# Optimization experiments

Hardware: AMD Instinct MI355X
Metric: run time of the kernel (lower is better)

Reference implementation:

```python
import jax, jax.numpy as jnp
import numpy as np

EPS = 1e-7
INF = 1e8
NUM_CLASSES = 80
SOFT_CENTER_RADIUS = 3.0
TOPK = 13
IOU_WEIGHT = 3.0
ALPHA = 1.0
BETA = 6.0
IMG = 640.0


def pairwise_iou(b1, b2):
    # b1: (B,N,4), b2: (B,M,4) in xyxy -> (B,N,M) IoU (mmdet BboxOverlaps2D, eps=1e-6)
    a1 = (b1[..., 2] - b1[..., 0]) * (b1[..., 3] - b1[..., 1])
    a2 = (b2[..., 2] - b2[..., 0]) * (b2[..., 3] - b2[..., 1])
    lt = jnp.maximum(b1[:, :, None, :2], b2[:, None, :, :2])
    rb = jnp.minimum(b1[:, :, None, 2:], b2[:, None, :, 2:])
    wh = jnp.clip(rb - lt, 0.0)
    inter = wh[..., 0] * wh[..., 1]
    union = a1[:, :, None] + a2[:, None, :] - inter
    return inter / jnp.maximum(union, 1e-6)


def _forward(pred_bboxes, pred_scores, priors, gt_labels, gt_bboxes, pad_bbox_flag):
    B, P, _ = pred_bboxes.shape
    G = gt_bboxes.shape[1]
    dt = pred_bboxes.dtype
    labels = gt_labels[..., 0]            # (B,G) int
    pad = pad_bbox_flag[..., 0]           # (B,G) float
    prior_xy = priors[:, :2]              # (P,2)
    strides = priors[:, 2]                # (P,)

    # ---- inside-gt test (find_inside_points, box_dim=4): (B,P,G) bool
    lt_ = prior_xy[None, :, None, :] - gt_bboxes[:, None, :, :2]
    rb_ = gt_bboxes[:, None, :, 2:] - prior_xy[None, :, None, :]
    is_in_gts = jnp.minimum(lt_.min(-1), rb_.min(-1)) > 0        # (B,P,G)
    is_in_gts_f = is_in_gts.astype(dt) * pad[:, None, :]         # masked by pad flag
    valid_mask = is_in_gts_f.sum(-1) > 0                          # (B,P)

    # ---- get_pos_mask (TaskAligned metric top-k) -> fg_mask_pre_prior
    overlaps = pairwise_iou(gt_bboxes, pred_bboxes)               # (B,G,P)
    scores_sig = jax.nn.sigmoid(pred_scores)                      # (B,P,C)
    scores_g = jnp.take_along_axis(scores_sig.transpose(0, 2, 1), labels[:, :, None], axis=1)  # (B,G,P)
    align = (scores_g ** ALPHA) * (overlaps ** BETA)              # (B,G,P)
    in_gts_gp = is_in_gts.transpose(0, 2, 1).astype(dt)           # (B,G,P)
    metrics = align * in_gts_gp
    _, topk_idxs = jax.lax.top_k(metrics, TOPK)                   # (B,G,TOPK)
    bb = jnp.arange(B)[:, None, None]
    gg = jnp.arange(G)[None, :, None]
    cnt = jnp.zeros((B, G, P), dt).at[bb, gg, topk_idxs].add(1.0)
    cnt = cnt * pad[:, :, None]
    is_in_topk = jnp.where(cnt > 1, 0.0, cnt)
    pos_mask = is_in_topk * in_gts_gp * pad[:, :, None]           # (B,G,P)
    # select_highest_overlaps: resolve priors matched to >1 gt via max IoU
    fg_pre = pos_mask.sum(1)                                      # (B,P)
    max_gt = overlaps.argmax(1)                                   # (B,P)
    is_max = (jnp.arange(G)[None, None, :] == max_gt[:, :, None]).astype(dt)  # (B,P,G)
    pos_mask = jnp.where((fg_pre > 1)[:, None, :], is_max.transpose(0, 2, 1), pos_mask)
    fg_mask_pre_prior = pos_mask.sum(1) > 0                       # (B,P) bool

    # ---- soft center prior
    gt_center = (gt_bboxes[..., :2] + gt_bboxes[..., 2:]) / 2.0   # (B,G,2)
    dist = jnp.sqrt(((prior_xy[None, :, None, :] - gt_center[:, None, :, :]) ** 2).sum(-1)) \
           / strides[None, :, None]                               # (B,P,G)
    dist = dist * valid_mask[..., None]
    soft_center_prior = jnp.power(10.0, dist - SOFT_CENTER_RADIUS)

    # ---- IoU cost
    pairwise_ious = pairwise_iou(pred_bboxes, gt_bboxes)          # (B,P,G)
    iou_cost = -jnp.log(pairwise_ious + EPS) * IOU_WEIGHT

    # ---- soft classification cost (QFL-style)
    logits = jnp.take_along_axis(pred_scores.transpose(0, 2, 1), labels[:, :, None], axis=1)
    logits = logits.transpose(0, 2, 1)                            # (B,P,G)
    scale = pairwise_ious - jax.nn.sigmoid(logits)
    bce = jnp.logaddexp(0.0, logits) - logits * pairwise_ious     # BCEWithLogits(logits, ious)
    cls_cost = bce * scale ** 2

    cost = cls_cost + iou_cost + soft_center_prior
    cost = jnp.where(valid_mask[..., None], cost, INF)            # (B,P,G)

    # ---- dynamic-k matching
    topk_ious, _ = jax.lax.top_k(pairwise_ious.transpose(0, 2, 1), TOPK)  # (B,G,TOPK)
    dynamic_ks = jnp.maximum(topk_ious.sum(-1).astype(jnp.int32), 1)      # (B,G)
    num_gts = pad.sum(-1).astype(jnp.int32)                                # (B,)
    sorted_idx = jnp.argsort(cost, axis=1)                                 # (B,P,G)
    ranks = jnp.arange(P)[None, :, None]
    gt_valid = jnp.arange(G)[None, :] < num_gts[:, None]                   # (B,G)
    sel = (ranks < dynamic_ks[:, None, :]) & gt_valid[:, None, :]          # (B,P,G), in sorted order
    bb2 = jnp.arange(B)[:, None, None]
    gg2 = jnp.arange(G)[None, None, :]
    matching = jnp.zeros((B, P, G), dt).at[bb2, sorted_idx, gg2].set(sel.astype(dt))
    multi = matching.sum(-1) > 1                                           # (B,P)
    argmin = cost.argmin(-1)                                               # (B,P)
    onehot_min = (jnp.arange(G)[None, None, :] == argmin[:, :, None]).astype(dt)
    matching = jnp.where(multi[..., None], onehot_min, matching)
    fg = matching.sum(-1) > 0                                              # (B,P)
    matched_ious = (matching * pairwise_ious).sum(-1)                      # (B,P)
    matched_gt_inds = matching.argmax(-1)                                  # (B,P)

    # ---- dense outputs (torch scatters into full-size tensors; same values here)
    assigned_labels = jnp.where(fg, jnp.take_along_axis(labels, matched_gt_inds, axis=1), NUM_CLASSES)
    assigned_labels_weights = jnp.ones((B, P), dt)
    assigned_bboxes = jnp.where(fg[..., None],
                                jnp.take_along_axis(gt_bboxes, matched_gt_inds[..., None].repeat(4, -1), axis=1),
                                0.0)
    assign_metrics = jnp.where(fg, matched_ious, 0.0)
    return assigned_labels, assigned_labels_weights, assigned_bboxes, assign_metrics, fg_mask_pre_prior


def setup_inputs() -> dict:
    key = jax.random.key(0)
    ks = jax.random.split(key, 6)
    B, G, C = 16, 100, 80
    # priors: anchor-free grid for 640x640, strides (8,16,32) -> P = 8400
    grids = []
    for s in (8, 16, 32):
        n = 640 // s
        xs = (np.arange(n, dtype=np.float32) + 0.5) * s
        yy, xx = np.meshgrid(xs, xs, indexing='ij')
        g = np.stack([xx.ravel(), yy.ravel(),
                      np.full(n * n, s, np.float32), np.full(n * n, s, np.float32)], -1)
        grids.append(g)
    priors = jnp.asarray(np.concatenate(grids, 0), jnp.float32)  # (8400, 4)
    P = priors.shape[0]

    def rand_boxes(k, shape):
        kc, kw = jax.random.split(k)
        cxy = jax.random.uniform(kc, shape + (2,), minval=0.0, maxval=IMG)
        wh = jax.random.uniform(kw, shape + (2,), minval=8.0, maxval=256.0)
        lt = jnp.clip(cxy - wh / 2, 0.0, IMG)
        rb = jnp.clip(cxy + wh / 2, 0.0, IMG)
        return jnp.concatenate([lt, rb], -1)

    pred_bboxes = rand_boxes(ks[0], (B, P))
    pred_scores = jax.random.normal(ks[1], (B, P, C), jnp.float32) * 2.0 - 2.0
    gt_bboxes = rand_boxes(ks[2], (B, G))
    gt_labels = jax.random.randint(ks[3], (B, G, 1), 0, C)
    n_valid = jax.random.randint(ks[4], (B,), 1, G + 1)
    pad_bbox_flag = (jnp.arange(G)[None, :] < n_valid[:, None]).astype(jnp.float32)[..., None]
    return {"pred_bboxes": pred_bboxes, "pred_scores": pred_scores, "priors": priors,
            "gt_labels": gt_labels, "gt_bboxes": gt_bboxes, "pad_bbox_flag": pad_bbox_flag}


def reference(pred_bboxes, pred_scores, priors, gt_labels, gt_bboxes, pad_bbox_flag):
    return _forward(pred_bboxes, pred_scores, priors, gt_labels, gt_bboxes, pad_bbox_flag)
```

## Files before the change

kernel.cpp:

```cpp
#include <hip/hip_runtime.h>
#include <cstdint>
#include <climits>
#include <cstddef>

#define TK 13
#define MAXG 128
#define CAP 192
#define NW 4
#define MCAP 24576

__device__ __forceinline__ float iou_fn(const float4 pb, const float4 gb){
  float pa = (pb.z - pb.x) * (pb.w - pb.y);
  float ga = (gb.z - gb.x) * (gb.w - gb.y);
  float ltx = fmaxf(pb.x, gb.x), lty = fmaxf(pb.y, gb.y);
  float rbx = fminf(pb.z, gb.z), rby = fminf(pb.w, gb.w);
  float w = fmaxf(rbx - ltx, 0.0f), h = fmaxf(rby - lty, 0.0f);
  float inter = w * h;
  float uni = pa + ga - inter;
  return inter / fmaxf(uni, 1e-6f);
}

__device__ __forceinline__ float sigmoid_f(float x){ return 1.0f / (1.0f + expf(-x)); }

__device__ __forceinline__ float cost_full(float iou, float s, float dist){
  float sig = sigmoid_f(s);
  float iouc = -logf(iou + 1e-7f) * 3.0f;
  float scale = iou - sig;
  float bce = fmaxf(s, 0.0f) + log1pf(expf(-fabsf(s))) - s * iou;
  float cls = bce * scale * scale;
  float soft = powf(10.0f, dist - 3.0f);
  return cls + iouc + soft;
}

__device__ __forceinline__ void bfly_max_u64(unsigned long long &v, int &l){
  #pragma unroll
  for (int off = 32; off >= 1; off >>= 1){
    unsigned long long ov = __shfl_xor(v, off);
    int ol = __shfl_xor(l, off);
    if (ov > v){ v = ov; l = ol; }
  }
}

__device__ __forceinline__ unsigned long long squeeze13(unsigned long long* buf, int& cnt, int lane){
  unsigned long long e0 = (lane < cnt) ? buf[lane] : 0ull;
  unsigned long long e1 = (lane + 64 < cnt) ? buf[lane + 64] : 0ull;
  unsigned long long e2 = (lane + 128 < cnt) ? buf[lane + 128] : 0ull;
  if (e0 < e2){ unsigned long long t = e0; e0 = e2; e2 = t; }
  if (e0 < e1){ unsigned long long t = e0; e0 = e1; e1 = t; }
  if (e1 < e2){ unsigned long long t = e1; e1 = e2; e2 = t; }
  unsigned long long T = 0;
  for (int r = 0; r < TK; ++r){
    unsigned long long m = e0; int l = lane;
    bfly_max_u64(m, l);
    if (lane == 0) buf[r] = m;
    T = m;
    if (lane == l){ e0 = e1; e1 = e2; e2 = 0ull; }
  }
  cnt = TK;
  return T;
}

__global__ __launch_bounds__(256) void k_valid(
    const float4* __restrict__ priors, const float4* __restrict__ gtb,
    const float* __restrict__ pad, unsigned long long* __restrict__ vmask,
    unsigned int* __restrict__ acc, unsigned int* __restrict__ mcnt,
    int P, int G, int nCh)
{
  int b = blockIdx.y;
  int p = blockIdx.x * 256 + threadIdx.x;
  if (b == 0 && p == 0) *mcnt = 0u;
  __shared__ float4 sg[MAXG];
  __shared__ float sp[MAXG];
  for (int i = threadIdx.x; i < G; i += 256){ sg[i] = gtb[b*G + i]; sp[i] = pad[b*G + i]; }
  __syncthreads();
  if (p >= P) return;
  float4 pr = priors[p];
  bool v = false;
  #pragma unroll 4
  for (int g = 0; g < G; ++g){
    float4 gb = sg[g];
    bool ig = (pr.x > gb.x) && (pr.y > gb.y) && (gb.z > pr.x) && (gb.w > pr.y);
    v = v || (ig && sp[g] > 0.5f);
  }
  size_t o = (size_t)b * P + p;
  acc[o] = 0u;
  unsigned long long m = __ballot(v);
  if ((threadIdx.x & 63) == 0) vmask[(size_t)b * nCh + (p >> 6)] = m;
}

__global__ __launch_bounds__(256) void k_scan(
    const float4* __restrict__ pred_bboxes, const float* __restrict__ pred_scores,
    const float4* __restrict__ priors, const int* __restrict__ gt_labels,
    const float4* __restrict__ gtbb, const float* __restrict__ pad,
    const unsigned long long* __restrict__ vmask,
    unsigned int* __restrict__ acc, unsigned int* __restrict__ mcnt,
    unsigned int* __restrict__ mlist,
    int P, int G, int C, int nCh)
{
  int bg = blockIdx.x;
  if (pad[bg] <= 0.5f) return;
  int b = bg / G;
  int g = bg - b * G;
  int tid = threadIdx.x;
  int lane = tid & 63;
  int wv = tid >> 6;
  float4 gb = gtbb[bg];
  int lbl = gt_labels[bg];
  float gcx = (gb.x + gb.z) * 0.5f, gcy = (gb.y + gb.w) * 0.5f;
  size_t bP = (size_t)b * P;
  const unsigned long long* vmb = vmask + (size_t)b * nCh;

  __shared__ unsigned long long bufM[NW*CAP], bufC[NW*CAP], bufI[NW*CAP];
  __shared__ unsigned int shwC, shwM, shwI;
  if (tid == 0){ shwC = 0xFFFFFFFFu; shwM = 0u; shwI = 0u; }
  __syncthreads();
  unsigned long long* bM = bufM + wv*CAP;
  unsigned long long* bC = bufC + wv*CAP;
  unsigned long long* bI = bufI + wv*CAP;

  int cntM = 0, cntC = 0, cntI = 0;
  int zM = 0, zC = 0;
  unsigned long long Tm = 0ull, Tc = 0ull;
  unsigned long long Ti = 0x00000000FFFFFFFFull;
  unsigned cbits = 0xFFFFFFFFu, mBbits = 0u, iBb = 0u;
  float thr = 1e30f, mB = 0.0f;
  unsigned long long laneLT = (1ull << lane) - 1ull;

  int p = wv * 64 + lane;
  bool inb = p < P;
  float4 pr = make_float4(0,0,0,0), pb = pr; bool vb = false;
  if (inb){
    pr = priors[p]; pb = pred_bboxes[bP + p]; vb = (vmb[wv] >> lane) & 1ull;
  }
  for (int c = wv; c < nCh; c += NW){
    int cn = c + NW;
    int pn = cn * 64 + lane;
    bool inbn = (cn < nCh) && (pn < P);
    float4 prn = make_float4(0,0,0,0), pbn = prn; bool vbn = false;
    if (inbn){
      prn = priors[pn]; pbn = pred_bboxes[bP + pn]; vbn = (vmb[cn] >> (pn & 63)) & 1ull;
    }
    { unsigned sC = shwC; if (sC < cbits){ cbits = sC;
        thr = 3.0f + log10f(__uint_as_float(cbits) * 1.00002f + 1e-6f); } }
    { unsigned sM = shwM; if (sM > mBbits){ mBbits = sM; mB = __uint_as_float(sM); } }
    { unsigned sI = shwI; if (sI > iBb) iBb = sI; }
    float iou = iou_fn(pb, gb);
    bool ig = inb && (pr.x > gb.x) && (pr.y > gb.y) && (gb.z > pr.x) && (gb.w > pr.y);
    bool pos = ig && (iou > 0.0f);
    unsigned long long keyI = ((unsigned long long)__float_as_uint(iou) << 32) | (unsigned)p;
    bool candI = inb && (keyI > Ti) && !((unsigned)(keyI >> 32) < iBb);
    float i2 = iou * iou;
    float bnd = (i2 * i2) * i2 * 1.000002f;
    bool needm = pos && !(bnd < mB);
    float dist = 0.0f; bool needc = false;
    if (vb){
      float dx = pr.x - gcx, dy = pr.y - gcy;
      dist = sqrtf(dx*dx + dy*dy) / pr.z;
      needc = !(dist > thr);
    }
    float sc = 0.0f;
    if (needm || needc) sc = pred_scores[(bP + p) * C + lbl];
    unsigned long long keyM = 0;
    if (__ballot(needm)){
      float met = sigmoid_f(sc) * powf(iou, 6.0f);
      if (needm)
        keyM = ((unsigned long long)__float_as_uint(met) << 32)
             | (unsigned)~(unsigned)((p << 1) | 1);
    }
    if (zM < TK && inb && !pos)
      keyM = (unsigned long long)(unsigned)~(unsigned)((p << 1) | (ig ? 1 : 0));
    bool candM = (keyM != 0ull) && (keyM > Tm) && !((unsigned)(keyM >> 32) < mBbits);
    unsigned long long keyC = 0;
    if (zC < TK && inb && !vb)
      keyC = ~(((unsigned long long)__float_as_uint(1e8f) << 32) | (unsigned)p);
    if (__ballot(needc)){
      float cst = cost_full(iou, sc, dist);
      if (needc)
        keyC = ~(((unsigned long long)__float_as_uint(cst) << 32) | (unsigned)p);
    }
    bool candC = (keyC != 0ull) && (keyC > Tc) && !((unsigned)((~keyC) >> 32) > cbits);
    if (cntI > CAP - 64){
      Ti = squeeze13(bI, cntI, lane);
      unsigned ib = (unsigned)(Ti >> 32);
      if (ib > iBb) iBb = ib;
      if (lane == 0 && ib) atomicMax(&shwI, ib);
      candI = candI && (keyI > Ti) && !((unsigned)(keyI >> 32) < iBb);
    }
    { unsigned long long mk = __ballot(candI);
      if (mk){ int off = cntI + __popcll(mk & laneLT); if (candI) bI[off] = keyI; cntI += __popcll(mk); } }
    if (cntM > CAP - 64){
      Tm = squeeze13(bM, cntM, lane);
      unsigned tb = (unsigned)(Tm >> 32);
      if (tb > mBbits){ mBbits = tb; mB = __uint_as_float(tb); }
      if (lane == 0 && tb) atomicMax(&shwM, tb);
      candM = candM && (keyM > Tm) && !((unsigned)(keyM >> 32) < mBbits);
    }
    { unsigned long long mk = __ballot(candM);
      if (mk){
        int off = cntM + __popcll(mk & laneLT);
        if (candM) bM[off] = keyM;
        cntM += __popcll(mk);
        unsigned long long zk = __ballot(candM && !pos);
        zM += __popcll(zk);
      } }
    if (cntC > CAP - 64){
      Tc = squeeze13(bC, cntC, lane);
      unsigned cb = (unsigned)((~Tc) >> 32);
      if (cb < cbits){ cbits = cb;
        thr = 3.0f + log10f(__uint_as_float(cbits) * 1.00002f + 1e-6f); }
      if (lane == 0) atomicMin(&shwC, cb);
      candC = candC && (keyC > Tc) && !((unsigned)((~keyC) >> 32) > cbits);
    }
    { unsigned long long mk = __ballot(candC);
      if (mk){
        int off = cntC + __popcll(mk & laneLT);
        if (candC) bC[off] = keyC;
        cntC += __popcll(mk);
        unsigned long long zk = __ballot(candC && !vb);
        zC += __popcll(zk);
      } }

    p = pn; inb = inbn; pr = prn; pb = pbn; vb = vbn;
  }

  squeeze13(bI, cntI, lane);
  squeeze13(bM, cntM, lane);
  squeeze13(bC, cntC, lane);
  __syncthreads();
  if (wv != 0) return;

  int w13 = lane / TK, r13 = lane - w13 * TK;
  int kd;
  {
    unsigned long long e = (lane < NW*TK) ? bufI[w13*CAP + r13] : 0ull;
    float ksum = 0.0f;
    for (int r = 0; r < TK; ++r){
      unsigned long long m = e; int l = lane;
      bfly_max_u64(m, l);
      ksum += __uint_as_float((unsigned)(m >> 32));
      if (lane == l) e = 0ull;
    }
    kd = (int)ksum; if (kd < 1) kd = 1;
  }
  {
    unsigned long long e = (lane < NW*TK) ? bufM[w13*CAP + r13] : 0ull;
    for (int r = 0; r < TK; ++r){
      unsigned long long m = e; int l = lane;
      bfly_max_u64(m, l);
      if (lane == 0 && m != 0ull){
        unsigned ix = ~(unsigned)(m & 0xFFFFFFFFull);
        if (ix & 1u) atomicOr(&acc[bP + (ix >> 1)], 2u);
      }
      if (lane == l) e = 0ull;
    }
  }
  {
    unsigned long long e = (lane < NW*TK) ? bufC[w13*CAP + r13] : 0ull;
    for (int r = 0; r < kd; ++r){
      unsigned long long m = e; int l = lane;
      bfly_max_u64(m, l);
      if (lane == 0 && m != 0ull){
        unsigned pp = (unsigned)((~m) & 0xFFFFFFFFull);
        unsigned old = atomicAdd(&acc[bP + pp], (1u << 17) | ((unsigned)g << 2));
        if ((old >> 17) == 1u){
          unsigned mi = atomicAdd(mcnt, 1u);
          if (mi < MCAP) mlist[mi] = (unsigned)(bP + pp);
        }
      }
      if (lane == l) e = 0ull;
    }
  }
}

__global__ __launch_bounds__(256) void k_final(
    const float4* __restrict__ pred_bboxes, const int* __restrict__ gt_labels,
    const float4* __restrict__ gtb, const unsigned int* __restrict__ acc,
    float* __restrict__ out, int B, int P, int G)
{
  int b = blockIdx.y;
  int p = blockIdx.x * 256 + threadIdx.x;
  __shared__ float4 sg[MAXG];
  __shared__ int sl[MAXG];
  for (int i = threadIdx.x; i < G; i += 256){
    sg[i] = gtb[b*G + i]; sl[i] = gt_labels[b*G + i];
  }
  __syncthreads();
  if (p >= P) return;
  size_t o = (size_t)b * P + p;
  unsigned int w = acc[o];
  int cnt = (int)(w >> 17);
  bool fg = cnt > 0;
  int mg = (cnt == 1) ? (int)((w >> 2) & 0x7FFFu) : 0;
  float4 pb = pred_bboxes[o];
  size_t BP = (size_t)B * P;
  out[o] = fg ? (float)sl[mg] : 80.0f;
  out[BP + o] = 1.0f;
  float4 ob = fg ? sg[mg] : make_float4(0.f, 0.f, 0.f, 0.f);
  ((float4*)(out + 2*BP))[o] = ob;
  out[6*BP + o] = fg ? iou_fn(pb, sg[mg]) : 0.0f;
  out[7*BP + o] = ((w >> 1) & 1u) ? 1.0f : 0.0f;
}

__global__ __launch_bounds__(256) void k_multi(
    const float4* __restrict__ pred_bboxes, const float* __restrict__ pred_scores,
    const float4* __restrict__ priors, const int* __restrict__ gt_labels,
    const float4* __restrict__ gtb, const unsigned long long* __restrict__ vmask,
    const unsigned int* __restrict__ mcnt, const unsigned int* __restrict__ mlist,
    float* __restrict__ out, int B, int P, int G, int C, int nCh)
{
  unsigned n = *mcnt; if (n > MCAP) n = MCAP;
  int lane = threadIdx.x & 63;
  int wid = (blockIdx.x * (blockDim.x >> 6)) + (threadIdx.x >> 6);
  int nw = gridDim.x * (blockDim.x >> 6);
  size_t BP = (size_t)B * P;
  for (unsigned i = wid; i < n; i += nw){
    unsigned o = mlist[i];
    int b = o / P;
    int p = o - b * P;
    float4 pb = pred_bboxes[o];
    bool vld = (vmask[(size_t)b * nCh + (p >> 6)] >> (p & 63)) & 1ull;
    int mg = 0;
    if (vld){
      float4 pr = priors[p];
      const float* srow = pred_scores + (size_t)o * C;
      unsigned long long best = 0xFFFFFFFFFFFFFFFFull;
      for (int g0 = lane; g0 < G; g0 += 64){
        float4 gbx = gtb[b*G + g0];
        float iou = iou_fn(pb, gbx);
        float s = srow[gt_labels[b*G + g0]];
        float gcx = (gbx.x + gbx.z) * 0.5f, gcy = (gbx.y + gbx.w) * 0.5f;
        float dx = pr.x - gcx, dy = pr.y - gcy;
        float dist = sqrtf(dx*dx + dy*dy) / pr.z;
        float cc = cost_full(iou, s, dist);
        unsigned long long k = ((unsigned long long)__float_as_uint(cc) << 32) | (unsigned)g0;
        if (k < best) best = k;
      }
      #pragma unroll
      for (int off = 32; off >= 1; off >>= 1){
        unsigned long long ov = __shfl_xor(best, off);
        if (ov < best) best = ov;
      }
      mg = (int)(best & 0xFFFFFFFFull);
    }
    if (lane == 0){
      float4 gbx = gtb[b*G + mg];
      out[o] = (float)gt_labels[b*G + mg];
      ((float4*)(out + 2*BP))[o] = gbx;
      out[6*BP + o] = iou_fn(pb, gbx);
    }
  }
}

extern "C" void kernel_launch(void* const* d_in, const int* in_sizes, int n_in,
                              void* d_out, int out_size, void* d_ws, size_t ws_size,
                              hipStream_t stream)
{
  const float4* pred_bboxes = (const float4*)d_in[0];
  const float*  pred_scores = (const float*)d_in[1];
  const float4* priors      = (const float4*)d_in[2];
  const int*    gt_labels   = (const int*)d_in[3];
  const float4* gt_bboxes   = (const float4*)d_in[4];
  const float*  pad         = (const float*)d_in[5];
  int P = in_sizes[2] / 4;
  int B = in_sizes[0] / (P * 4);
  int C = in_sizes[1] / (B * P);
  int G = in_sizes[4] / (B * 4);
  int BG = B * G;
  int nCh = (P + 63) >> 6;

  uint8_t* ws = (uint8_t*)d_ws;
  size_t accOff  = (size_t)B * nCh * 8;
  size_t mcntOff = accOff + (size_t)B * P * 4;
  mcntOff = (mcntOff + 15) & ~(size_t)15;
  size_t mlistOff = mcntOff + 16;

  unsigned long long* vmask = (unsigned long long*)ws;
  unsigned int* acc   = (unsigned int*)(ws + accOff);
  unsigned int* mcnt  = (unsigned int*)(ws + mcntOff);
  unsigned int* mlist = (unsigned int*)(ws + mlistOff);
  float* out = (float*)d_out;

  dim3 gridA((P + 255) / 256, B);
  k_valid<<<gridA, 256, 0, stream>>>(priors, gt_bboxes, pad, vmask, acc, mcnt, P, G, nCh);
  k_scan<<<BG, NW*64, 0, stream>>>(pred_bboxes, pred_scores,
                                   priors, gt_labels, gt_bboxes, pad, vmask,
                                   acc, mcnt, mlist, P, G, C, nCh);
  k_final<<<gridA, 256, 0, stream>>>(pred_bboxes, gt_labels, gt_bboxes, acc, out, B, P, G);
  k_multi<<<64, 256, 0, stream>>>(pred_bboxes, pred_scores, priors, gt_labels, gt_bboxes,
                                  vmask, mcnt, mlist, out, B, P, G, C, nCh);
}
```

Measured before the change: 275.8 us.

## Double waves per gt block in scan kernel and merge with two-candidate lanes

Raises the scan kernel's block to 512 threads (8 waves) so each gt's prior range is split across twice as many waves. The final top-k merge now holds two candidate entries per lane to cover the 8×13 partial results. Early break is added when no candidates remain. This aims to shorten the per-gt serial scan at the cost of larger blocks, more shared memory for the per-wave buffers, and a larger merge.

Result: slower. 297.3 us (+7.8%).

```diff
diff --git a/kernel.cpp b/kernel.cpp
--- a/kernel.cpp
+++ b/kernel.cpp
@@ -6,7 +6,7 @@
 #define TK 13
 #define MAXG 128
 #define CAP 192
-#define NW 4
+#define NW 8
 #define MCAP 24576
 
 __device__ __forceinline__ float iou_fn(const float4 pb, const float4 gb){
@@ -88,7 +88,7 @@
   if ((threadIdx.x & 63) == 0) vmask[(size_t)b * nCh + (p >> 6)] = m;
 }
 
-__global__ __launch_bounds__(256) void k_scan(
+__global__ __launch_bounds__(512) void k_scan(
     const float4* __restrict__ pred_bboxes, const float* __restrict__ pred_scores,
     const float4* __restrict__ priors, const int* __restrict__ gt_labels,
     const float4* __restrict__ gtbb, const float* __restrict__ pad,
@@ -229,37 +229,44 @@
   __syncthreads();
   if (wv != 0) return;
 
-  int w13 = lane / TK, r13 = lane - w13 * TK;
+  int i0 = lane, i1 = lane + 64;
+  int w0 = i0 / TK, r0 = i0 - w0 * TK;
+  int w1 = i1 / TK, r1 = i1 - w1 * TK;
   int kd;
   {
-    unsigned long long e = (lane < NW*TK) ? bufI[w13*CAP + r13] : 0ull;
+    unsigned long long e0 = (i0 < NW*TK) ? bufI[w0*CAP + r0] : 0ull;
+    unsigned long long e1 = (i1 < NW*TK) ? bufI[w1*CAP + r1] : 0ull;
     float ksum = 0.0f;
     for (int r = 0; r < TK; ++r){
-      unsigned long long m = e; int l = lane;
+      unsigned long long m = e0 > e1 ? e0 : e1; int l = lane;
       bfly_max_u64(m, l);
       ksum += __uint_as_float((unsigned)(m >> 32));
-      if (lane == l) e = 0ull;
+      if (lane == l){ if (e0 == m) e0 = 0ull; else e1 = 0ull; }
     }
     kd = (int)ksum; if (kd < 1) kd = 1;
   }
   {
-    unsigned long long e = (lane < NW*TK) ? bufM[w13*CAP + r13] : 0ull;
+    unsigned long long e0 = (i0 < NW*TK) ? bufM[w0*CAP + r0] : 0ull;
+    unsigned long long e1 = (i1 < NW*TK) ? bufM[w1*CAP + r1] : 0ull;
     for (int r = 0; r < TK; ++r){
-      unsigned long long m = e; int l = lane;
+      unsigned long long m = e0 > e1 ? e0 : e1; int l = lane;
       bfly_max_u64(m, l);
-      if (lane == 0 && m != 0ull){
+      if (m == 0ull) break;
+      if (lane == 0){
         unsigned ix = ~(unsigned)(m & 0xFFFFFFFFull);
         if (ix & 1u) atomicOr(&acc[bP + (ix >> 1)], 2u);
       }
-      if (lane == l) e = 0ull;
+      if (lane == l){ if (e0 == m) e0 = 0ull; else e1 = 0ull; }
     }
   }
   {
-    unsigned long long e = (lane < NW*TK) ? bufC[w13*CAP + r13] : 0ull;
+    unsigned long long e0 = (i0 < NW*TK) ? bufC[w0*CAP + r0] : 0ull;
+    unsigned long long e1 = (i1 < NW*TK) ? bufC[w1*CAP + r1] : 0ull;
     for (int r = 0; r < kd; ++r){
-      unsigned long long m = e; int l = lane;
+      unsigned long long m = e0 > e1 ? e0 : e1; int l = lane;
       bfly_max_u64(m, l);
-      if (lane == 0 && m != 0ull){
+      if (m == 0ull) break;
+      if (lane == 0){
         unsigned pp = (unsigned)((~m) & 0xFFFFFFFFull);
         unsigned old = atomicAdd(&acc[bP + pp], (1u << 17) | ((unsigned)g << 2));
         if ((old >> 17) == 1u){
@@ -267,7 +274,7 @@
           if (mi < MCAP) mlist[mi] = (unsigned)(bP + pp);
         }
       }
-      if (lane == l) e = 0ull;
+      if (lane == l){ if (e0 == m) e0 = 0ull; else e1 = 0ull; }
     }
   }
 }
```

## Skip whole prior chunks via per-chunk bounding boxes; fold multi-assign into final kernel

Applied to the files above, without the earlier changes.

k_valid now also stores a per-64-prior bounding box of the predicted boxes and of the prior centres, plus the chunk stride. k_scan uses these boxes to skip whole chunks that cannot overlap the gt box or fall below the current top-k cost and metric thresholds, so it loads fewer predictions, priors and scores. The separate k_multi kernel and its global list are removed. Priors matched to several gts are resolved in k_final with a nearest-centre seed and a lower-bound prune on the distance cost. This adds bound computations and more divergent work in k_final, and relies on the pruning bounds being conservative.

After: 362.1 us. +31.3%, slower.

```diff
diff --git a/kernel.cpp b/kernel.cpp
--- a/kernel.cpp
+++ b/kernel.cpp
@@ -7,7 +7,6 @@
 #define MAXG 128
 #define CAP 192
 #define NW 4
-#define MCAP 24576
 
 __device__ __forceinline__ float iou_fn(const float4 pb, const float4 gb){
   float pa = (pb.z - pb.x) * (pb.w - pb.y);
@@ -61,31 +60,51 @@
 }
 
 __global__ __launch_bounds__(256) void k_valid(
-    const float4* __restrict__ priors, const float4* __restrict__ gtb,
-    const float* __restrict__ pad, unsigned long long* __restrict__ vmask,
-    unsigned int* __restrict__ acc, unsigned int* __restrict__ mcnt,
+    const float4* __restrict__ priors, const float4* __restrict__ pred_bboxes,
+    const float4* __restrict__ gtb, const float* __restrict__ pad,
+    unsigned long long* __restrict__ vmask, unsigned int* __restrict__ acc,
+    float4* __restrict__ predAB, float4* __restrict__ prAB, float* __restrict__ strC,
     int P, int G, int nCh)
 {
   int b = blockIdx.y;
   int p = blockIdx.x * 256 + threadIdx.x;
-  if (b == 0 && p == 0) *mcnt = 0u;
   __shared__ float4 sg[MAXG];
   __shared__ float sp[MAXG];
   for (int i = threadIdx.x; i < G; i += 256){ sg[i] = gtb[b*G + i]; sp[i] = pad[b*G + i]; }
   __syncthreads();
-  if (p >= P) return;
-  float4 pr = priors[p];
+  int lane = threadIdx.x & 63;
+  int ch = p >> 6;
+  bool inb = p < P;
+  float4 pr = inb ? priors[p] : make_float4(0,0,0,0);
+  float4 pb = inb ? pred_bboxes[(size_t)b*P + p] : make_float4(0,0,0,0);
   bool v = false;
-  #pragma unroll 4
-  for (int g = 0; g < G; ++g){
-    float4 gb = sg[g];
-    bool ig = (pr.x > gb.x) && (pr.y > gb.y) && (gb.z > pr.x) && (gb.w > pr.y);
-    v = v || (ig && sp[g] > 0.5f);
-  }
-  size_t o = (size_t)b * P + p;
-  acc[o] = 0u;
+  if (inb){
+    #pragma unroll 4
+    for (int g = 0; g < G; ++g){
+      float4 gb = sg[g];
+      bool ig = (pr.x > gb.x) && (pr.y > gb.y) && (gb.z > pr.x) && (gb.w > pr.y);
+      v = v || (ig && sp[g] > 0.5f);
+    }
+    acc[(size_t)b * P + p] = 0u;
+  }
   unsigned long long m = __ballot(v);
-  if ((threadIdx.x & 63) == 0) vmask[(size_t)b * nCh + (p >> 6)] = m;
+  if (lane == 0 && ch < nCh) vmask[(size_t)b * nCh + ch] = m;
+  float inf = __builtin_inff();
+  float x1 = inb ? pb.x : inf,  y1 = inb ? pb.y : inf;
+  float x2 = inb ? pb.z : -inf, y2 = inb ? pb.w : -inf;
+  float px1 = inb ? pr.x : inf,  py1 = inb ? pr.y : inf;
+  float px2 = inb ? pr.x : -inf, py2 = inb ? pr.y : -inf;
+  #pragma unroll
+  for (int off = 32; off >= 1; off >>= 1){
+    x1 = fminf(x1, __shfl_xor(x1, off));  y1 = fminf(y1, __shfl_xor(y1, off));
+    x2 = fmaxf(x2, __shfl_xor(x2, off));  y2 = fmaxf(y2, __shfl_xor(y2, off));
+    px1 = fminf(px1, __shfl_xor(px1, off)); py1 = fminf(py1, __shfl_xor(py1, off));
+    px2 = fmaxf(px2, __shfl_xor(px2, off)); py2 = fmaxf(py2, __shfl_xor(py2, off));
+  }
+  if (lane == 0 && ch < nCh){
+    predAB[(size_t)b * nCh + ch] = make_float4(x1, y1, x2, y2);
+    if (b == 0){ prAB[ch] = make_float4(px1, py1, px2, py2); strC[ch] = pr.z; }
+  }
 }
 
 __global__ __launch_bounds__(256) void k_scan(
@@ -93,9 +112,9 @@
     const float4* __restrict__ priors, const int* __restrict__ gt_labels,
     const float4* __restrict__ gtbb, const float* __restrict__ pad,
     const unsigned long long* __restrict__ vmask,
-    unsigned int* __restrict__ acc, unsigned int* __restrict__ mcnt,
-    unsigned int* __restrict__ mlist,
-    int P, int G, int C, int nCh)
+    const float4* __restrict__ predAB, const float4* __restrict__ prAB,
+    const float* __restrict__ strC,
+    unsigned int* __restrict__ acc, int P, int G, int C, int nCh)
 {
   int bg = blockIdx.x;
   if (pad[bg] <= 0.5f) return;
@@ -109,6 +128,8 @@
   float gcx = (gb.x + gb.z) * 0.5f, gcy = (gb.y + gb.w) * 0.5f;
   size_t bP = (size_t)b * P;
   const unsigned long long* vmb = vmask + (size_t)b * nCh;
+  const float4* pAB = predAB + (size_t)b * nCh;
+  const unsigned B1E8 = __float_as_uint(1e8f);
 
   __shared__ unsigned long long bufM[NW*CAP], bufC[NW*CAP], bufI[NW*CAP];
   __shared__ unsigned int shwC, shwM, shwI;
@@ -126,101 +147,111 @@
   float thr = 1e30f, mB = 0.0f;
   unsigned long long laneLT = (1ull << lane) - 1ull;
 
-  int p = wv * 64 + lane;
-  bool inb = p < P;
-  float4 pr = make_float4(0,0,0,0), pb = pr; bool vb = false;
-  if (inb){
-    pr = priors[p]; pb = pred_bboxes[bP + p]; vb = (vmb[wv] >> lane) & 1ull;
-  }
+  float4 pA = pAB[wv];
+  float4 rA = prAB[wv];
+  float strc = strC[wv];
   for (int c = wv; c < nCh; c += NW){
     int cn = c + NW;
-    int pn = cn * 64 + lane;
-    bool inbn = (cn < nCh) && (pn < P);
-    float4 prn = make_float4(0,0,0,0), pbn = prn; bool vbn = false;
-    if (inbn){
-      prn = priors[pn]; pbn = pred_bboxes[bP + pn]; vbn = (vmb[cn] >> (pn & 63)) & 1ull;
-    }
+    float4 pAn = pA, rAn = rA; float strn = strc;
+    if (cn < nCh){ pAn = pAB[cn]; rAn = prAB[cn]; strn = strC[cn]; }
     { unsigned sC = shwC; if (sC < cbits){ cbits = sC;
         thr = 3.0f + log10f(__uint_as_float(cbits) * 1.00002f + 1e-6f); } }
     { unsigned sM = shwM; if (sM > mBbits){ mBbits = sM; mB = __uint_as_float(sM); } }
     { unsigned sI = shwI; if (sI > iBb) iBb = sI; }
-    float iou = iou_fn(pb, gb);
-    bool ig = inb && (pr.x > gb.x) && (pr.y > gb.y) && (gb.z > pr.x) && (gb.w > pr.y);
-    bool pos = ig && (iou > 0.0f);
-    unsigned long long keyI = ((unsigned long long)__float_as_uint(iou) << 32) | (unsigned)p;
-    bool candI = inb && (keyI > Ti) && !((unsigned)(keyI >> 32) < iBb);
-    float i2 = iou * iou;
-    float bnd = (i2 * i2) * i2 * 1.000002f;
-    bool needm = pos && !(bnd < mB);
-    float dist = 0.0f; bool needc = false;
-    if (vb){
-      float dx = pr.x - gcx, dy = pr.y - gcy;
-      dist = sqrtf(dx*dx + dy*dy) / pr.z;
-      needc = !(dist > thr);
-    }
-    float sc = 0.0f;
-    if (needm || needc) sc = pred_scores[(bP + p) * C + lbl];
-    unsigned long long keyM = 0;
-    if (__ballot(needm)){
-      float met = sigmoid_f(sc) * powf(iou, 6.0f);
-      if (needm)
-        keyM = ((unsigned long long)__float_as_uint(met) << 32)
-             | (unsigned)~(unsigned)((p << 1) | 1);
-    }
-    if (zM < TK && inb && !pos)
-      keyM = (unsigned long long)(unsigned)~(unsigned)((p << 1) | (ig ? 1 : 0));
-    bool candM = (keyM != 0ull) && (keyM > Tm) && !((unsigned)(keyM >> 32) < mBbits);
-    unsigned long long keyC = 0;
-    if (zC < TK && inb && !vb)
-      keyC = ~(((unsigned long long)__float_as_uint(1e8f) << 32) | (unsigned)p);
-    if (__ballot(needc)){
-      float cst = cost_full(iou, sc, dist);
-      if (needc)
-        keyC = ~(((unsigned long long)__float_as_uint(cst) << 32) | (unsigned)p);
-    }
-    bool candC = (keyC != 0ull) && (keyC > Tc) && !((unsigned)((~keyC) >> 32) > cbits);
-    if (cntI > CAP - 64){
-      Ti = squeeze13(bI, cntI, lane);
-      unsigned ib = (unsigned)(Ti >> 32);
-      if (ib > iBb) iBb = ib;
-      if (lane == 0 && ib) atomicMax(&shwI, ib);
-      candI = candI && (keyI > Ti) && !((unsigned)(keyI >> 32) < iBb);
-    }
-    { unsigned long long mk = __ballot(candI);
-      if (mk){ int off = cntI + __popcll(mk & laneLT); if (candI) bI[off] = keyI; cntI += __popcll(mk); } }
-    if (cntM > CAP - 64){
-      Tm = squeeze13(bM, cntM, lane);
-      unsigned tb = (unsigned)(Tm >> 32);
-      if (tb > mBbits){ mBbits = tb; mB = __uint_as_float(tb); }
-      if (lane == 0 && tb) atomicMax(&shwM, tb);
-      candM = candM && (keyM > Tm) && !((unsigned)(keyM >> 32) < mBbits);
-    }
-    { unsigned long long mk = __ballot(candM);
-      if (mk){
-        int off = cntM + __popcll(mk & laneLT);
-        if (candM) bM[off] = keyM;
-        cntM += __popcll(mk);
-        unsigned long long zk = __ballot(candM && !pos);
-        zM += __popcll(zk);
-      } }
-    if (cntC > CAP - 64){
-      Tc = squeeze13(bC, cntC, lane);
-      unsigned cb = (unsigned)((~Tc) >> 32);
-      if (cb < cbits){ cbits = cb;
-        thr = 3.0f + log10f(__uint_as_float(cbits) * 1.00002f + 1e-6f); }
-      if (lane == 0) atomicMin(&shwC, cb);
-      candC = candC && (keyC > Tc) && !((unsigned)((~keyC) >> 32) > cbits);
-    }
-    { unsigned long long mk = __ballot(candC);
-      if (mk){
-        int off = cntC + __popcll(mk & laneLT);
-        if (candC) bC[off] = keyC;
-        cntC += __popcll(mk);
-        unsigned long long zk = __ballot(candC && !vb);
-        zC += __popcll(zk);
-      } }
-
-    p = pn; inb = inbn; pr = prn; pb = pbn; vb = vbn;
+    bool geoI = !(pA.x < gb.z && pA.z > gb.x && pA.y < gb.w && pA.w > gb.y);
+    bool geoM = !(rA.z > gb.x && rA.x < gb.z && rA.w > gb.y && rA.y < gb.w);
+    float dxr = fmaxf(0.0f, fmaxf(rA.x - gcx, gcx - rA.z));
+    float dyr = fmaxf(0.0f, fmaxf(rA.y - gcy, gcy - rA.w));
+    float drr = sqrtf(dxr*dxr + dyr*dyr) / strc;
+    bool poolM = (zM >= TK) || (mBbits > 0u);
+    bool poolC = (zC >= TK) || (cbits < B1E8);
+    bool skipMt = geoM && poolM;
+    bool skipCt = (drr > thr) && poolC;
+    if (!(geoI && skipMt && skipCt)){
+      int p = c * 64 + lane;
+      bool inb = p < P;
+      float4 pb = inb ? pred_bboxes[bP + p] : make_float4(0,0,0,0);
+      float iou = iou_fn(pb, gb);
+      unsigned long long keyI = ((unsigned long long)__float_as_uint(iou) << 32) | (unsigned)p;
+      bool candI = inb && (keyI > Ti) && !((unsigned)(keyI >> 32) < iBb);
+      if (cntI > CAP - 64){
+        Ti = squeeze13(bI, cntI, lane);
+        unsigned ib = (unsigned)(Ti >> 32);
+        if (ib > iBb) iBb = ib;
+        if (lane == 0 && ib) atomicMax(&shwI, ib);
+        candI = candI && (keyI > Ti) && !((unsigned)(keyI >> 32) < iBb);
+      }
+      { unsigned long long mk = __ballot(candI);
+        if (mk){ int off = cntI + __popcll(mk & laneLT); if (candI) bI[off] = keyI; cntI += __popcll(mk); } }
+      if (!(skipMt && skipCt)){
+        float4 pr = inb ? priors[p] : make_float4(0,0,0,0);
+        bool vb = inb && (((vmb[c] >> lane) & 1ull) != 0ull);
+        bool ig = inb && (pr.x > gb.x) && (pr.y > gb.y) && (gb.z > pr.x) && (gb.w > pr.y);
+        bool pos = ig && (iou > 0.0f);
+        float i2 = iou * iou;
+        float bnd = (i2 * i2) * i2 * 1.000002f;
+        bool needm = pos && !(bnd < mB);
+        float dist = 0.0f; bool needc = false;
+        if (vb){
+          float dx = pr.x - gcx, dy = pr.y - gcy;
+          dist = sqrtf(dx*dx + dy*dy) / pr.z;
+          needc = !(dist > thr);
+        }
+        float sc = 0.0f;
+        if (needm || needc) sc = pred_scores[(bP + p) * C + lbl];
+        unsigned long long keyM = 0;
+        if (__ballot(needm)){
+          float met = sigmoid_f(sc) * powf(iou, 6.0f);
+          if (needm)
+            keyM = ((unsigned long long)__float_as_uint(met) << 32)
+                 | (unsigned)~(unsigned)((p << 1) | 1);
+        }
+        if (zM < TK && inb && !pos)
+          keyM = (unsigned long long)(unsigned)~(unsigned)((p << 1) | (ig ? 1 : 0));
+        bool candM = (keyM != 0ull) && (keyM > Tm) && !((unsigned)(keyM >> 32) < mBbits);
+        unsigned long long keyC = 0;
+        if (zC < TK && inb && !vb)
+          keyC = ~(((unsigned long long)__float_as_uint(1e8f) << 32) | (unsigned)p);
+        if (__ballot(needc)){
+          float cst = cost_full(iou, sc, dist);
+          if (needc)
+            keyC = ~(((unsigned long long)__float_as_uint(cst) << 32) | (unsigned)p);
+        }
+        bool candC = (keyC != 0ull) && (keyC > Tc) && !((unsigned)((~keyC) >> 32) > cbits);
+        if (cntM > CAP - 64){
+          Tm = squeeze13(bM, cntM, lane);
+          unsigned tb = (unsigned)(Tm >> 32);
+          if (tb > mBbits){ mBbits = tb; mB = __uint_as_float(tb); }
+          if (lane == 0 && tb) atomicMax(&shwM, tb);
+          candM = candM && (keyM > Tm) && !((unsigned)(keyM >> 32) < mBbits);
+        }
+        { unsigned long long mk = __ballot(candM);
+          if (mk){
+            int off = cntM + __popcll(mk & laneLT);
+            if (candM) bM[off] = keyM;
+            cntM += __popcll(mk);
+            unsigned long long zk = __ballot(candM && !pos);
+            zM += __popcll(zk);
+          } }
+        if (cntC > CAP - 64){
+          Tc = squeeze13(bC, cntC, lane);
+          unsigned cb = (unsigned)((~Tc) >> 32);
+          if (cb < cbits){ cbits = cb;
+            thr = 3.0f + log10f(__uint_as_float(cbits) * 1.00002f + 1e-6f); }
+          if (lane == 0) atomicMin(&shwC, cb);
+          candC = candC && (keyC > Tc) && !((unsigned)((~keyC) >> 32) > cbits);
+        }
+        { unsigned long long mk = __ballot(candC);
+          if (mk){
+            int off = cntC + __popcll(mk & laneLT);
+            if (candC) bC[off] = keyC;
+            cntC += __popcll(mk);
+            unsigned long long zk = __ballot(candC && !vb);
+            zC += __popcll(zk);
+          } }
+      }
+    }
+    pA = pAn; rA = rAn; strc = strn;
   }
 
   squeeze13(bI, cntI, lane);
@@ -247,7 +278,8 @@
     for (int r = 0; r < TK; ++r){
       unsigned long long m = e; int l = lane;
       bfly_max_u64(m, l);
-      if (lane == 0 && m != 0ull){
+      if (m == 0ull) break;
+      if (lane == 0){
         unsigned ix = ~(unsigned)(m & 0xFFFFFFFFull);
         if (ix & 1u) atomicOr(&acc[bP + (ix >> 1)], 2u);
       }
@@ -259,13 +291,10 @@
     for (int r = 0; r < kd; ++r){
       unsigned long long m = e; int l = lane;
       bfly_max_u64(m, l);
-      if (lane == 0 && m != 0ull){
+      if (m == 0ull) break;
+      if (lane == 0){
         unsigned pp = (unsigned)((~m) & 0xFFFFFFFFull);
-        unsigned old = atomicAdd(&acc[bP + pp], (1u << 17) | ((unsigned)g << 2));
-        if ((old >> 17) == 1u){
-          unsigned mi = atomicAdd(mcnt, 1u);
-          if (mi < MCAP) mlist[mi] = (unsigned)(bP + pp);
-        }
+        atomicAdd(&acc[bP + pp], (1u << 17) | ((unsigned)g << 2));
       }
       if (lane == l) e = 0ull;
     }
@@ -273,16 +302,21 @@
 }
 
 __global__ __launch_bounds__(256) void k_final(
-    const float4* __restrict__ pred_bboxes, const int* __restrict__ gt_labels,
-    const float4* __restrict__ gtb, const unsigned int* __restrict__ acc,
-    float* __restrict__ out, int B, int P, int G)
+    const float4* __restrict__ pred_bboxes, const float* __restrict__ pred_scores,
+    const float4* __restrict__ priors, const int* __restrict__ gt_labels,
+    const float4* __restrict__ gtb, const unsigned long long* __restrict__ vmask,
+    const unsigned int* __restrict__ acc, float* __restrict__ out,
+    int B, int P, int G, int C, int nCh)
 {
   int b = blockIdx.y;
   int p = blockIdx.x * 256 + threadIdx.x;
   __shared__ float4 sg[MAXG];
   __shared__ int sl[MAXG];
+  __shared__ float2 sc[MAXG];
   for (int i = threadIdx.x; i < G; i += 256){
-    sg[i] = gtb[b*G + i]; sl[i] = gt_labels[b*G + i];
+    float4 gbx = gtb[b*G + i];
+    sg[i] = gbx; sl[i] = gt_labels[b*G + i];
+    sc[i] = make_float2((gbx.x + gbx.z) * 0.5f, (gbx.y + gbx.w) * 0.5f);
   }
   __syncthreads();
   if (p >= P) return;
@@ -290,8 +324,37 @@
   unsigned int w = acc[o];
   int cnt = (int)(w >> 17);
   bool fg = cnt > 0;
-  int mg = (cnt == 1) ? (int)((w >> 2) & 0x7FFFu) : 0;
+  int mg = 0;
   float4 pb = pred_bboxes[o];
+  if (cnt == 1){
+    mg = (int)((w >> 2) & 0x7FFFu);
+  } else if (cnt > 1){
+    bool vld = (vmask[(size_t)b * nCh + (p >> 6)] >> (p & 63)) & 1ull;
+    if (vld){
+      float4 pr = priors[p];
+      const float* srow = pred_scores + o * C;
+      float bd2 = __builtin_inff(); int gd = 0;
+      for (int gg = 0; gg < G; ++gg){
+        float dx = pr.x - sc[gg].x, dy = pr.y - sc[gg].y;
+        float d2 = dx*dx + dy*dy;
+        if (d2 < bd2){ bd2 = d2; gd = gg; }
+      }
+      float dxs = pr.x - sc[gd].x, dys = pr.y - sc[gd].y;
+      float ds0 = sqrtf(dxs*dxs + dys*dys) / pr.z;
+      float bestc = cost_full(iou_fn(pb, sg[gd]), srow[sl[gd]], ds0);
+      mg = gd;
+      for (int gg = 0; gg < G; ++gg){
+        float dxx = pr.x - sc[gg].x, dyy = pr.y - sc[gg].y;
+        float dd = sqrtf(dxx*dxx + dyy*dyy) / pr.z;
+        float lb = exp2f((dd - 3.0f) * 3.321928f) * 0.9999f - 1e-6f;
+        if (lb > bestc) continue;
+        float cc = cost_full(iou_fn(pb, sg[gg]), srow[sl[gg]], dd);
+        if (cc < bestc || (cc == bestc && gg < mg)){ bestc = cc; mg = gg; }
+      }
+    } else {
+      mg = 0;
+    }
+  }
   size_t BP = (size_t)B * P;
   out[o] = fg ? (float)sl[mg] : 80.0f;
   out[BP + o] = 1.0f;
@@ -299,56 +362,6 @@
   ((float4*)(out + 2*BP))[o] = ob;
   out[6*BP + o] = fg ? iou_fn(pb, sg[mg]) : 0.0f;
   out[7*BP + o] = ((w >> 1) & 1u) ? 1.0f : 0.0f;
-}
-
-__global__ __launch_bounds__(256) void k_multi(
-    const float4* __restrict__ pred_bboxes, const float* __restrict__ pred_scores,
-    const float4* __restrict__ priors, const int* __restrict__ gt_labels,
-    const float4* __restrict__ gtb, const unsigned long long* __restrict__ vmask,
-    const unsigned int* __restrict__ mcnt, const unsigned int* __restrict__ mlist,
-    float* __restrict__ out, int B, int P, int G, int C, int nCh)
-{
-  unsigned n = *mcnt; if (n > MCAP) n = MCAP;
-  int lane = threadIdx.x & 63;
-  int wid = (blockIdx.x * (blockDim.x >> 6)) + (threadIdx.x >> 6);
-  int nw = gridDim.x * (blockDim.x >> 6);
-  size_t BP = (size_t)B * P;
-  for (unsigned i = wid; i < n; i += nw){
-    unsigned o = mlist[i];
-    int b = o / P;
-    int p = o - b * P;
-    float4 pb = pred_bboxes[o];
-    bool vld = (vmask[(size_t)b * nCh + (p >> 6)] >> (p & 63)) & 1ull;
-    int mg = 0;
-    if (vld){
-      float4 pr = priors[p];
-      const float* srow = pred_scores + (size_t)o * C;
-      unsigned long long best = 0xFFFFFFFFFFFFFFFFull;
-      for (int g0 = lane; g0 < G; g0 += 64){
-        float4 gbx = gtb[b*G + g0];
-        float iou = iou_fn(pb, gbx);
-        float s = srow[gt_labels[b*G + g0]];
-        float gcx = (gbx.x + gbx.z) * 0.5f, gcy = (gbx.y + gbx.w) * 0.5f;
-        float dx = pr.x - gcx, dy = pr.y - gcy;
-        float dist = sqrtf(dx*dx + dy*dy) / pr.z;
-        float cc = cost_full(iou, s, dist);
-        unsigned long long k = ((unsigned long long)__float_as_uint(cc) << 32) | (unsigned)g0;
-        if (k < best) best = k;
-      }
-      #pragma unroll
-      for (int off = 32; off >= 1; off >>= 1){
-        unsigned long long ov = __shfl_xor(best, off);
-        if (ov < best) best = ov;
-      }
-      mg = (int)(best & 0xFFFFFFFFull);
-    }
-    if (lane == 0){
-      float4 gbx = gtb[b*G + mg];
-      out[o] = (float)gt_labels[b*G + mg];
-      ((float4*)(out + 2*BP))[o] = gbx;
-      out[6*BP + o] = iou_fn(pb, gbx);
-    }
-  }
 }
 
 extern "C" void kernel_launch(void* const* d_in, const int* in_sizes, int n_in,
@@ -369,23 +382,21 @@
   int nCh = (P + 63) >> 6;
 
   uint8_t* ws = (uint8_t*)d_ws;
-  size_t accOff  = (size_t)B * nCh * 8;
-  size_t mcntOff = accOff + (size_t)B * P * 4;
-  mcntOff = (mcntOff + 15) & ~(size_t)15;
-  size_t mlistOff = mcntOff + 16;
-
-  unsigned long long* vmask = (unsigned long long*)ws;
-  unsigned int* acc   = (unsigned int*)(ws + accOff);
-  unsigned int* mcnt  = (unsigned int*)(ws + mcntOff);
-  unsigned int* mlist = (unsigned int*)(ws + mlistOff);
+  size_t off = 0;
+  unsigned long long* vmask = (unsigned long long*)(ws + off); off += (size_t)B * nCh * 8;
+  unsigned int* acc = (unsigned int*)(ws + off);               off += (size_t)B * P * 4;
+  off = (off + 15) & ~(size_t)15;
+  float4* predAB = (float4*)(ws + off);                        off += (size_t)B * nCh * 16;
+  float4* prAB = (float4*)(ws + off);                          off += (size_t)nCh * 16;
+  float* strC = (float*)(ws + off);                            off += (size_t)nCh * 4;
   float* out = (float*)d_out;
 
   dim3 gridA((P + 255) / 256, B);
-  k_valid<<<gridA, 256, 0, stream>>>(priors, gt_bboxes, pad, vmask, acc, mcnt, P, G, nCh);
-  k_scan<<<BG, NW*64, 0, stream>>>(pred_bboxes, pred_scores,
-                                   priors, gt_labels, gt_bboxes, pad, vmask,
-                                   acc, mcnt, mlist, P, G, C, nCh);
-  k_final<<<gridA, 256, 0, stream>>>(pred_bboxes, gt_labels, gt_bboxes, acc, out, B, P, G);
-  k_multi<<<64, 256, 0, stream>>>(pred_bboxes, pred_scores, priors, gt_labels, gt_bboxes,
-                                  vmask, mcnt, mlist, out, B, P, G, C, nCh);
-}
+  k_valid<<<gridA, 256, 0, stream>>>(priors, pred_bboxes, gt_bboxes, pad,
+                                     vmask, acc, predAB, prAB, strC, P, G, nCh);
+  k_scan<<<BG, NW*64, 0, stream>>>(pred_bboxes, pred_scores, priors, gt_labels,
+                                   gt_bboxes, pad, vmask, predAB, prAB, strC,
+                                   acc, P, G, C, nCh);
+  k_final<<<gridA, 256, 0, stream>>>(pred_bboxes, pred_scores, priors, gt_labels,
+                                     gt_bboxes, vmask, acc, out, B, P, G, C, nCh);
+}
```
